# Kernel tuning notes

Hardware: AMD Instinct MI355X
Metric: run time of the kernel (lower is better)

## Reference

```python
import jax, jax.numpy as jnp
import numpy as np

B, INP, C, N, D, H = 512, 512, 1024, 256, 128, 8


def setup_inputs() -> dict:
    key = jax.random.key(0)
    ks = iter(jax.random.split(key, 40))
    rn = lambda shape, s=1.0: jax.random.normal(next(ks), shape, jnp.float32) * s
    d = {}
    d['x'] = rn((B, INP))
    d['h1'] = rn((B, C), 0.1)
    d['c1'] = rn((B, C), 0.1)
    d['h2'] = rn((B, C), 0.1)
    d['c2'] = rn((B, C), 0.1)
    d['w_prev'] = jax.nn.softmax(rn((B, H, N)), axis=-1)  # valid address dist (unused by math)
    d['r_prev'] = rn((B, H, D))
    d['M_prev'] = rn((B, N, D))
    s = 0.02
    d['W_ih1'] = rn((4 * C, INP + H * D), s); d['W_hh1'] = rn((4 * C, C), s)
    d['b_ih1'] = rn((4 * C,), s); d['b_hh1'] = rn((4 * C,), s)
    d['W_ih2'] = rn((4 * C, C), s); d['W_hh2'] = rn((4 * C, C), s)
    d['b_ih2'] = rn((4 * C,), s); d['b_hh2'] = rn((4 * C,), s)
    d['W_rk'] = rn((H * D, C), s); d['b_rk'] = rn((H * D,), s)
    d['W_wk'] = rn((H * D, C), s); d['b_wk'] = rn((H * D,), s)
    d['W_rb'] = rn((H, C), s); d['b_rb'] = rn((H,), s)
    d['W_wb'] = rn((H, C), s); d['b_wb'] = rn((H,), s)
    d['W_er'] = rn((H * D, C), s); d['b_er'] = rn((H * D,), s)
    d['W_ad'] = rn((H * D, C), s); d['b_ad'] = rn((H * D,), s)
    d['W_sh'] = rn((H * 3, C), s); d['b_sh'] = rn((H * 3,), s)
    d['W_ga'] = rn((H, C), s); d['b_ga'] = rn((H,), s)
    return d


def _lstm_cell(inp, h, c, Wih, Whh, bih, bhh):
    g = inp @ Wih.T + bih + h @ Whh.T + bhh
    i, f, gg, o = jnp.split(g, 4, axis=-1)  # torch LSTMCell gate order
    c_new = jax.nn.sigmoid(f) * c + jax.nn.sigmoid(i) * jnp.tanh(gg)
    return jax.nn.sigmoid(o) * jnp.tanh(c_new), c_new


def _normalize(v):
    n = jnp.linalg.norm(v, axis=-1, keepdims=True)
    return v / jnp.maximum(n, 1e-12)


def _content_weights(M, K, beta):
    cos = jnp.einsum('bnd,bhd->bhn', _normalize(M), _normalize(K))
    return jax.nn.softmax(beta[..., None] * cos, axis=-1)


def reference(x, h1, c1, h2, c2, w_prev, r_prev, M_prev,
              W_ih1, W_hh1, b_ih1, b_hh1, W_ih2, W_hh2, b_ih2, b_hh2,
              W_rk, b_rk, W_wk, b_wk, W_rb, b_rb, W_wb, b_wb,
              W_er, b_er, W_ad, b_ad, W_sh, b_sh, W_ga, b_ga):
    Bsz = x.shape[0]
    inp = jnp.concatenate([x, r_prev.reshape(Bsz, -1)], axis=-1)
    h1n, c1n = _lstm_cell(inp, h1, c1, W_ih1, W_hh1, b_ih1, b_hh1)
    h2n, c2n = _lstm_cell(h1n, h2, c2, W_ih2, W_hh2, b_ih2, b_hh2)  # dropout = eval identity
    RK = (h2n @ W_rk.T + b_rk).reshape(Bsz, H, D)
    WK = (h2n @ W_wk.T + b_wk).reshape(Bsz, H, D)
    Br = jax.nn.softplus(h2n @ W_rb.T + b_rb)
    Bw = jax.nn.softplus(h2n @ W_wb.T + b_wb)
    erase = jax.nn.sigmoid(h2n @ W_er.T + b_er).reshape(Bsz, H, D)
    addv = jnp.tanh(h2n @ W_ad.T + b_ad).reshape(Bsz, H, D)
    shifts = (h2n @ W_sh.T + b_sh).reshape(Bsz, H, 3)
    gamma = h2n @ W_ga.T + b_ga
    # write
    w_w = _content_weights(M_prev, WK, Bw)                      # [B,H,N]
    w_ = w_w[..., None]                                         # [B,H,N,1]
    M = M_prev * (1.0 - jnp.sum(w_ * erase[:, :, None, :], axis=1)) \
        + jnp.sum(w_ * addv[:, :, None, :], axis=1)             # [B,N,D]
    # read: content -> shift -> sharpen
    w_r = _content_weights(M, RK, Br)
    rolls = jnp.stack([jnp.roll(w_r, -1, axis=-1), w_r, jnp.roll(w_r, 1, axis=-1)], axis=-1)
    w_s = jnp.einsum('bhnk,bhk->bhn', rolls, jax.nn.softmax(shifts, axis=-1))
    g = 1.0 + jax.nn.softplus(gamma)[..., None]
    w_g = w_s ** g
    w_r = w_g / (jnp.sum(w_g, axis=-1, keepdims=True) + 1e-12)
    r = jnp.einsum('bhn,bnd->bhd', w_r, M)
    return (h1n, c1n, h2n, c2n, w_r, r, M)
```

## Files before the change

### kernel.cpp

```cpp
#include <hip/hip_runtime.h>
#include <cstdint>
#include <cstddef>


typedef __attribute__((ext_vector_type(4))) float f32x4;
typedef __attribute__((ext_vector_type(8))) __bf16 bf16x8;
typedef __attribute__((ext_vector_type(4))) unsigned short u16x4;
typedef __attribute__((ext_vector_type(8))) unsigned short u16x8;

struct ASeg { const unsigned short* A; int ldA; int kt; };
struct WSeg { const float* W; int ldW; };

__device__ __forceinline__ unsigned short f2bf(float f) {
  return __builtin_bit_cast(unsigned short, (__bf16)f);
}
__device__ __forceinline__ float sigmoidf_(float x) { return 1.f / (1.f + expf(-x)); }
__device__ __forceinline__ float softplusf_(float x) {
  return fmaxf(x, 0.f) + log1pf(expf(-fabsf(x)));
}

__device__ __forceinline__ void xcd_decode(int& k, int& g) {
  int hid = blockIdx.x;
  int xcd = hid & 7, slot = hid >> 3;
  g = xcd + 8 * (slot >> 2);
  k = slot & 3;
}


__device__ __forceinline__ void stage_tile(
    unsigned short* lAb, unsigned short* lBb,
    const float* (*s_brow)[64],
    const unsigned short* A0, int ldA0, const unsigned short* A1, int ldA1,
    const unsigned short* A2, int ldA2, int b0, int b1, int kt, int t)
{
  int si; const unsigned short* A; int ldA; int ktl;
  if (kt < b0)      { si = 0; ktl = kt;      A = A0; ldA = ldA0; }
  else if (kt < b1) { si = 1; ktl = kt - b0; A = A1; ldA = ldA1; }
  else              { si = 2; ktl = kt - b1; A = A2; ldA = ldA2; }
  const int kl = ktl * 64;
  const int wave = t >> 6, lane = t & 63;
  const int a_r8 = lane >> 3;
  const int a_col = (((lane & 7) ^ a_r8) * 8);
#pragma unroll
  for (int q = 0; q < 4; ++q) {
    const int R = (wave * 4 + q) * 8;
    const unsigned short* src = A + (size_t)(R + a_r8) * ldA + kl + a_col;
    __builtin_amdgcn_global_load_lds(
        (const __attribute__((address_space(1))) void*)src,
        (__attribute__((address_space(3))) void*)(lAb + R * 64), 16, 0, 0);
  }
  const int brow0 = t >> 4, bseg = t & 15;
#pragma unroll
  for (int i = 0; i < 4; ++i) {
    const int row = brow0 + 16 * i;
    const float* wp = s_brow[si][row];
    f32x4 v = *(const f32x4*)(wp + kl + bseg * 4);
    u16x4 p; p.x = f2bf(v.x); p.y = f2bf(v.y); p.z = f2bf(v.z); p.w = f2bf(v.w);
    *(u16x4*)&lBb[row * 64 + ((bseg * 4) ^ ((row & 7) << 3))] = p;
  }
}

__device__ __forceinline__ void mfma_tile(const unsigned short* lAb,
                                          const unsigned short* lBb,
                                          int t, f32x4 (&acc)[2][4])
{
  const int wave = t >> 6, lane = t & 63;
  const int lr = lane & 15, lk = lane >> 4;
#pragma unroll
  for (int kk = 0; kk < 2; ++kk) {
    bf16x8 af[2], bfr[4];
#pragma unroll
    for (int mi = 0; mi < 2; ++mi) {
      const int ar = wave * 32 + mi * 16 + lr;
      af[mi] = *(const bf16x8*)&lAb[ar * 64 + ((kk * 32 + lk * 8) ^ ((ar & 7) << 3))];
    }
#pragma unroll
    for (int ni = 0; ni < 4; ++ni) {
      const int br = ni * 16 + lr;
      bfr[ni] = *(const bf16x8*)&lBb[br * 64 + ((kk * 32 + lk * 8) ^ ((br & 7) << 3))];
    }
#pragma unroll
    for (int mi = 0; mi < 2; ++mi)
#pragma unroll
      for (int ni = 0; ni < 4; ++ni)
        acc[mi][ni] = __builtin_amdgcn_mfma_f32_16x16x32_bf16(af[mi], bfr[ni], acc[mi][ni], 0, 0, 0);
  }
}

#define GEMM_PIPELINE(A0, LD0, A1, LD1, A2, LD2, B0, B1, TOTAL)                    \
  stage_tile(lA[0], lB[0], s_brow, A0, LD0, A1, LD1, A2, LD2, B0, B1, 0, t);       \
  __syncthreads();                                                                 \
  _Pragma("unroll 1")                                                              \
  for (int kt = 0; kt < (TOTAL); ++kt) {                                           \
    const int cur = kt & 1;                                                        \
    if (kt + 1 < (TOTAL))                                                          \
      stage_tile(lA[cur ^ 1], lB[cur ^ 1], s_brow, A0, LD0, A1, LD1, A2, LD2,      \
                 B0, B1, kt + 1, t);                                               \
    mfma_tile(lA[cur], lB[cur], t, acc);                                           \
    __syncthreads();                                                               \
  }

__global__ __launch_bounds__(256) void lstm_gemm(
    ASeg a0, ASeg a1, ASeg a2, WSeg w0, WSeg w1, WSeg w2,
    const float* __restrict__ bih, const float* __restrict__ bhh,
    const float* __restrict__ cprev,
    float* __restrict__ hout, float* __restrict__ cout,
    unsigned short* __restrict__ hb)
{
  __shared__ __align__(16) unsigned short lA[2][128 * 64];
  __shared__ __align__(16) unsigned short lB[2][64 * 64];
  __shared__ const float* s_brow[3][64];
  const int t = threadIdx.x;
  int k, g; xcd_decode(k, g);
  const int m0 = k * 128, j0 = g * 16;

  if (t < 192) {
    const int si = t >> 6, row = t & 63;
    const float* W = si == 0 ? w0.W : si == 1 ? w1.W : w2.W;
    const int ldW  = si == 0 ? w0.ldW : si == 1 ? w1.ldW : w2.ldW;
    if (W) s_brow[si][row] = W + (size_t)((row >> 4) * 1024 + j0 + (row & 15)) * ldW;
  }
  __syncthreads();

  f32x4 acc[2][4];
#pragma unroll
  for (int i = 0; i < 2; ++i)
#pragma unroll
    for (int j = 0; j < 4; ++j) acc[i][j] = (f32x4){0.f, 0.f, 0.f, 0.f};

  const unsigned short* A0 = a0.A + (size_t)m0 * a0.ldA;
  const unsigned short* A1 = a1.A + (size_t)m0 * a1.ldA;
  const unsigned short* A2 = a2.A ? a2.A + (size_t)m0 * a2.ldA : a0.A;
  const int b0 = a0.kt, b1 = b0 + a1.kt, total = b1 + a2.kt;
  GEMM_PIPELINE(A0, a0.ldA, A1, a1.ldA, A2, a2.ldA, b0, b1, total)

  const int lane = t & 63, wave = t >> 6;
  const int lr = lane & 15, lk = lane >> 4;
  const int j = j0 + lr;
  float bs0 = bih[j] + bhh[j];
  float bs1 = bih[1024 + j] + bhh[1024 + j];
  float bs2 = bih[2048 + j] + bhh[2048 + j];
  float bs3 = bih[3072 + j] + bhh[3072 + j];
#pragma unroll
  for (int mi = 0; mi < 2; ++mi) {
#pragma unroll
    for (int jp = 0; jp < 4; ++jp) {
      const int r = m0 + wave * 32 + mi * 16 + lk * 4 + jp;
      float gi = acc[mi][0][jp] + bs0;
      float gf = acc[mi][1][jp] + bs1;
      float gc = acc[mi][2][jp] + bs2;
      float go = acc[mi][3][jp] + bs3;
      float cp = cprev[(size_t)r * 1024 + j];
      float cn = sigmoidf_(gf) * cp + sigmoidf_(gi) * tanhf(gc);
      float hn = sigmoidf_(go) * tanhf(cn);
      cout[(size_t)r * 1024 + j] = cn;
      hout[(size_t)r * 1024 + j] = hn;
      hb[(size_t)r * 1024 + j] = f2bf(hn);
    }
  }
}

__global__ __launch_bounds__(256) void heads_gemm(
    const unsigned short* __restrict__ A,
    const float* W0, const float* W1, const float* W2, const float* W3,
    const float* bb0, const float* bb1, const float* bb2, const float* bb3,
    const float* W_rb, const float* b_rb, const float* W_wb, const float* b_wb,
    const float* W_sh, const float* b_sh, const float* W_ga, const float* b_ga,
    float* o0, float* o1, float* o2, float* o3,
    float* Brw, float* Bww, float* SHw, float* GAw)
{
  __shared__ __align__(16) unsigned short lA[2][128 * 64];
  __shared__ __align__(16) unsigned short lB[2][64 * 64];
  __shared__ const float* s_brow[3][64];
  const int t = threadIdx.x;
  const bool small = (blockIdx.x >= 256);
  int m0, n0 = 0, z = 4;
  if (!small) {
    int k, g; xcd_decode(k, g);
    m0 = k * 128; n0 = (g & 15) * 64; z = g >> 4;
  } else {
    m0 = (blockIdx.x - 256) * 128;
  }
  const float* W  = z == 0 ? W0 : z == 1 ? W1 : z == 2 ? W2 : z == 3 ? W3 : nullptr;
  const float* bb = z == 0 ? bb0 : z == 1 ? bb1 : z == 2 ? bb2 : bb3;
  float* o        = z == 0 ? o0 : z == 1 ? o1 : z == 2 ? o2 : o3;

  if (t < 64) {
    if (!small) {
      s_brow[0][t] = W + (size_t)(n0 + t) * 1024;
    } else {
      const float* p;
      if (t < 8)       p = W_rb + (size_t)t * 1024;
      else if (t < 16) p = W_wb + (size_t)(t - 8) * 1024;
      else if (t < 40) p = W_sh + (size_t)(t - 16) * 1024;
      else if (t < 48) p = W_ga + (size_t)(t - 40) * 1024;
      else             p = W_ga;
      s_brow[0][t] = p;
    }
  }
  __syncthreads();

  f32x4 acc[2][4];
#pragma unroll
  for (int i = 0; i < 2; ++i)
#pragma unroll
    for (int j = 0; j < 4; ++j) acc[i][j] = (f32x4){0.f, 0.f, 0.f, 0.f};

  const unsigned short* A0 = A + (size_t)m0 * 1024;
  GEMM_PIPELINE(A0, 1024, A0, 1024, A0, 1024, 16, 16, 16)

  const int lane = t & 63, wave = t >> 6;
  const int lr = lane & 15, lk = lane >> 4;
  if (!small) {
#pragma unroll
    for (int mi = 0; mi < 2; ++mi) {
#pragma unroll
      for (int ni = 0; ni < 4; ++ni) {
        const int col = n0 + ni * 16 + lr;
        const float bv = bb[col];
#pragma unroll
        for (int jp = 0; jp < 4; ++jp) {
          const int r = m0 + wave * 32 + mi * 16 + lk * 4 + jp;
          float v = acc[mi][ni][jp] + bv;
          if (z == 2) v = sigmoidf_(v);
          else if (z == 3) v = tanhf(v);
          o[(size_t)r * 1024 + col] = v;
        }
      }
    }
  } else {
#pragma unroll
    for (int mi = 0; mi < 2; ++mi) {
#pragma unroll
      for (int ni = 0; ni < 4; ++ni) {
        const int c = ni * 16 + lr;
#pragma unroll
        for (int jp = 0; jp < 4; ++jp) {
          const int r = m0 + wave * 32 + mi * 16 + lk * 4 + jp;
          const float v = acc[mi][ni][jp];
          if (c < 8)       Brw[r * 8 + c] = softplusf_(v + b_rb[c]);
          else if (c < 16) Bww[r * 8 + (c - 8)] = softplusf_(v + b_wb[c - 8]);
          else if (c < 40) SHw[(size_t)r * 24 + (c - 16)] = v + b_sh[c - 16];
          else if (c < 48) GAw[r * 8 + (c - 40)] = v + b_ga[c - 40];
        }
      }
    }
  }
}

__global__ __launch_bounds__(256) void cvt_bf16(
    const float* __restrict__ x, const float* __restrict__ rp,
    const float* __restrict__ h1, const float* __restrict__ h2,
    unsigned short* __restrict__ ob)
{
  const int i = blockIdx.x * 256 + threadIdx.x;
  const float* src; int off;
  if (i < 32768)       { src = x;  off = i; }
  else if (i < 98304)  { src = rp; off = i - 32768; }
  else if (i < 163840) { src = h1; off = i - 98304; }
  else                 { src = h2; off = i - 163840; }
  f32x4 a = *(const f32x4*)(src + (size_t)off * 8);
  f32x4 c = *(const f32x4*)(src + (size_t)off * 8 + 4);
  u16x8 p;
  p[0] = f2bf(a.x); p[1] = f2bf(a.y); p[2] = f2bf(a.z); p[3] = f2bf(a.w);
  p[4] = f2bf(c.x); p[5] = f2bf(c.y); p[6] = f2bf(c.z); p[7] = f2bf(c.w);
  *(u16x8*)(ob + (size_t)i * 8) = p;
}

__device__ __forceinline__ void cos_pass(const float* __restrict__ Mbase,
                                         const float (*s_k)[128],
                                         const float* s_scale, float (*s_w)[256],
                                         int b, int t)
{
  const int l8 = t & 7, rg = t >> 3;
  f32x4 kv0[8], kv1[8], kv2[8], kv3[8];
#pragma unroll
  for (int h = 0; h < 8; ++h) {
    kv0[h] = *(const f32x4*)&s_k[h][(l8 + 0) * 4];
    kv1[h] = *(const f32x4*)&s_k[h][(l8 + 8) * 4];
    kv2[h] = *(const f32x4*)&s_k[h][(l8 + 16) * 4];
    kv3[h] = *(const f32x4*)&s_k[h][(l8 + 24) * 4];
  }
#pragma unroll 1
  for (int j = 0; j < 8; ++j) {
    const int n = j * 32 + rg;
    const float* mr = Mbase + ((size_t)b * 256 + n) * 128;
    f32x4 v0 = *(const f32x4*)(mr + (l8 + 0) * 4);
    f32x4 v1 = *(const f32x4*)(mr + (l8 + 8) * 4);
    f32x4 v2 = *(const f32x4*)(mr + (l8 + 16) * 4);
    f32x4 v3 = *(const f32x4*)(mr + (l8 + 24) * 4);
    f32x4 sv = v0 * v0 + v1 * v1 + v2 * v2 + v3 * v3;
    float sq = sv.x + sv.y + sv.z + sv.w;
    float dot[8];
#pragma unroll
    for (int h = 0; h < 8; ++h) {
      f32x4 dv = v0 * kv0[h] + v1 * kv1[h] + v2 * kv2[h] + v3 * kv3[h];
      dot[h] = dv.x + dv.y + dv.z + dv.w;
    }
#pragma unroll
    for (int mk = 1; mk < 8; mk <<= 1) {
      sq += __shfl_xor(sq, mk, 64);
#pragma unroll
      for (int h = 0; h < 8; ++h) dot[h] += __shfl_xor(dot[h], mk, 64);
    }
    if (l8 == 0) {
      const float invM = 1.f / fmaxf(sqrtf(sq), 1e-12f);
#pragma unroll
      for (int h = 0; h < 8; ++h) s_w[h][n] = dot[h] * invM * s_scale[h];
    }
  }
}

__device__ __forceinline__ void softmax256(float (*s_w)[256], int t) {
  const int h = t >> 5, l32 = t & 31;
  float v[8]; float mx = -3.4e38f;
#pragma unroll
  for (int i = 0; i < 8; ++i) { v[i] = s_w[h][l32 + 32 * i]; mx = fmaxf(mx, v[i]); }
#pragma unroll
  for (int mk = 1; mk < 32; mk <<= 1) mx = fmaxf(mx, __shfl_xor(mx, mk, 64));
  float sum = 0.f;
#pragma unroll
  for (int i = 0; i < 8; ++i) { v[i] = expf(v[i] - mx); sum += v[i]; }
#pragma unroll
  for (int mk = 1; mk < 32; mk <<= 1) sum += __shfl_xor(sum, mk, 64);
  const float inv = 1.f / sum;
#pragma unroll
  for (int i = 0; i < 8; ++i) s_w[h][l32 + 32 * i] = v[i] * inv;
}

__global__ __launch_bounds__(256, 2) void ntm_rw(
    const float* __restrict__ Mp, const float* __restrict__ WK,
    const float* __restrict__ ER, const float* __restrict__ AD,
    const float* __restrict__ RK,
    const float* __restrict__ Bw, const float* __restrict__ Br,
    const float* __restrict__ SH, const float* __restrict__ GA,
    float* __restrict__ Mo, float* __restrict__ wr_o, float* __restrict__ r_o)
{
  const int b = blockIdx.x, t = threadIdx.x;
  __shared__ __align__(16) float s_wk[8][128], s_er[8][128], s_ad[8][128], s_rk[8][128];
  __shared__ __align__(16) float s_w[8][256], s_w2[8][256];
  __shared__ __align__(16) float s_part[8][8][128];
  __shared__ float s_scw[8], s_scr[8], s_sh3[8][3], s_g[8];

  {
    const int h = t >> 5, d16 = (t & 31) * 4;
    const size_t off = (size_t)b * 1024 + t * 4;
    *(f32x4*)&s_wk[h][d16] = *(const f32x4*)(WK + off);
    *(f32x4*)&s_er[h][d16] = *(const f32x4*)(ER + off);
    *(f32x4*)&s_ad[h][d16] = *(const f32x4*)(AD + off);
    *(f32x4*)&s_rk[h][d16] = *(const f32x4*)(RK + off);
  }
  __syncthreads();
  if (t < 64) {
    const int h = t >> 3, l8 = t & 7;
    f32x4 aw = {0,0,0,0}, ar = {0,0,0,0};
#pragma unroll
    for (int q = 0; q < 4; ++q) {
      f32x4 w = *(const f32x4*)&s_wk[h][(l8 + q * 8) * 4];
      f32x4 r = *(const f32x4*)&s_rk[h][(l8 + q * 8) * 4];
      aw += w * w; ar += r * r;
    }
    float sw = aw.x + aw.y + aw.z + aw.w;
    float sr = ar.x + ar.y + ar.z + ar.w;
#pragma unroll
    for (int mk = 1; mk < 8; mk <<= 1) {
      sw += __shfl_xor(sw, mk, 64); sr += __shfl_xor(sr, mk, 64);
    }
    if (l8 == 0) {
      s_scw[h] = Bw[b * 8 + h] / fmaxf(sqrtf(sw), 1e-12f);
      s_scr[h] = Br[b * 8 + h] / fmaxf(sqrtf(sr), 1e-12f);
    }
  }
  if (t < 8) {
    s_g[t] = 1.f + softplusf_(GA[b * 8 + t]);
    float s0 = SH[b * 24 + t * 3], s1 = SH[b * 24 + t * 3 + 1], s2 = SH[b * 24 + t * 3 + 2];
    float mx = fmaxf(s0, fmaxf(s1, s2));
    float e0 = expf(s0 - mx), e1 = expf(s1 - mx), e2 = expf(s2 - mx);
    float inv = 1.f / (e0 + e1 + e2);
    s_sh3[t][0] = e0 * inv; s_sh3[t][1] = e1 * inv; s_sh3[t][2] = e2 * inv;
  }
  __syncthreads();

  cos_pass(Mp, s_wk, s_scw, s_w, b, t);
  __syncthreads();
  softmax256(s_w, t);
  __syncthreads();

  {
    const int d16 = (t & 31) * 4;
    f32x4 er8[8], ad8[8];
#pragma unroll
    for (int h = 0; h < 8; ++h) {
      er8[h] = *(const f32x4*)&s_er[h][d16];
      ad8[h] = *(const f32x4*)&s_ad[h][d16];
    }
#pragma unroll 1
    for (int j = 0; j < 32; ++j) {
      const int idx = j * 256 + t;
      const int n = idx >> 5;
      f32x4 m = *(const f32x4*)(Mp + (size_t)b * 32768 + (size_t)idx * 4);
      f32x4 er = {0,0,0,0}, ad = {0,0,0,0};
#pragma unroll
      for (int h = 0; h < 8; ++h) {
        const float w = s_w[h][n];
        er += w * er8[h];
        ad += w * ad8[h];
      }
      f32x4 o;
#pragma unroll
      for (int e = 0; e < 4; ++e) o[e] = m[e] * (1.f - er[e]) + ad[e];
      *(f32x4*)(Mo + (size_t)b * 32768 + (size_t)idx * 4) = o;
    }
  }
  __syncthreads();

  cos_pass(Mo, s_rk, s_scr, s_w, b, t);
  __syncthreads();
  softmax256(s_w, t);
  __syncthreads();

  {
    const int h = t >> 5, l32 = t & 31;
    float vals[8]; float sum = 0.f;
#pragma unroll
    for (int i = 0; i < 8; ++i) {
      const int n = l32 + 32 * i;
      float ws = s_w[h][(n + 1) & 255] * s_sh3[h][0]
               + s_w[h][n] * s_sh3[h][1]
               + s_w[h][(n - 1) & 255] * s_sh3[h][2];
      float wg = powf(ws, s_g[h]);
      vals[i] = wg; sum += wg;
    }
#pragma unroll
    for (int mk = 1; mk < 32; mk <<= 1) sum += __shfl_xor(sum, mk, 64);
    const float inv = 1.f / (sum + 1e-12f);
#pragma unroll
    for (int i = 0; i < 8; ++i) {
      const int n = l32 + 32 * i;
      const float w = vals[i] * inv;
      s_w2[h][n] = w;
      wr_o[((size_t)b * 8 + h) * 256 + n] = w;
    }
  }
  __syncthreads();

  {
    const int gq = t >> 5;
    const int q = t & 31;
    f32x4 pr[8];
#pragma unroll
    for (int h = 0; h < 8; ++h) pr[h] = (f32x4){0,0,0,0};
#pragma unroll 1
    for (int j = 0; j < 32; ++j) {
      const int n = j * 8 + gq;
      f32x4 v = *(const f32x4*)(Mo + (size_t)b * 32768 + (size_t)n * 128 + q * 4);
#pragma unroll
      for (int h = 0; h < 8; ++h) pr[h] += s_w2[h][n] * v;
    }
#pragma unroll
    for (int h = 0; h < 8; ++h) *(f32x4*)&s_part[gq][h][q * 4] = pr[h];
  }
  __syncthreads();
  {
    const int h = t >> 5, q = t & 31;
    f32x4 a = (f32x4){0,0,0,0};
#pragma unroll
    for (int g2 = 0; g2 < 8; ++g2) a += *(const f32x4*)&s_part[g2][h][q * 4];
    *(f32x4*)(r_o + ((size_t)b * 8 + h) * 128 + q * 4) = a;
  }
}

extern "C" void kernel_launch(void* const* d_in, const int* in_sizes, int n_in,
                              void* d_out, int out_size, void* d_ws, size_t ws_size,
                              hipStream_t stream)
{
  const float* x      = (const float*)d_in[0];
  const float* h1     = (const float*)d_in[1];
  const float* c1     = (const float*)d_in[2];
  const float* h2     = (const float*)d_in[3];
  const float* c2     = (const float*)d_in[4];
  const float* r_prev = (const float*)d_in[6];
  const float* M_prev = (const float*)d_in[7];
  const float* W_ih1  = (const float*)d_in[8];
  const float* W_hh1  = (const float*)d_in[9];
  const float* b_ih1  = (const float*)d_in[10];
  const float* b_hh1  = (const float*)d_in[11];
  const float* W_ih2  = (const float*)d_in[12];
  const float* W_hh2  = (const float*)d_in[13];
  const float* b_ih2  = (const float*)d_in[14];
  const float* b_hh2  = (const float*)d_in[15];
  const float* W_rk   = (const float*)d_in[16];
  const float* b_rk   = (const float*)d_in[17];
  const float* W_wk   = (const float*)d_in[18];
  const float* b_wk   = (const float*)d_in[19];
  const float* W_rb   = (const float*)d_in[20];
  const float* b_rb   = (const float*)d_in[21];
  const float* W_wb   = (const float*)d_in[22];
  const float* b_wb   = (const float*)d_in[23];
  const float* W_er   = (const float*)d_in[24];
  const float* b_er   = (const float*)d_in[25];
  const float* W_ad   = (const float*)d_in[26];
  const float* b_ad   = (const float*)d_in[27];
  const float* W_sh   = (const float*)d_in[28];
  const float* b_sh   = (const float*)d_in[29];
  const float* W_ga   = (const float*)d_in[30];
  const float* b_ga   = (const float*)d_in[31];

  float* out = (float*)d_out;
  float* h1n = out;
  float* c1n = out + 524288;
  float* h2n = out + 1048576;
  float* c2n = out + 1572864;
  float* wro = out + 2097152;
  float* r_o = out + 3145728;
  float* M_o = out + 3670016;

  float* wsf = (float*)d_ws;
  float* RK  = wsf;
  float* WKb = RK + 524288;
  float* ER  = WKb + 524288;
  float* AD  = ER + 524288;
  float* Brb = AD + 524288;
  float* Bwb = Brb + 4096;
  float* SHb = Bwb + 4096;
  float* GAb = SHb + 12288;
  const size_t f32_need  = 2121728;
  const size_t bf16_need = 2883584;
  unsigned short* bfb;
  if (ws_size >= f32_need * 4 + bf16_need * 2) {
    bfb = (unsigned short*)(wsf + f32_need);
  } else {
    bfb = (unsigned short*)(M_o + (16777216 - (bf16_need + 1) / 2));
  }
  unsigned short* xb   = bfb;
  unsigned short* rb   = xb + 262144;
  unsigned short* h1b  = rb + 524288;
  unsigned short* h2b  = h1b + 524288;
  unsigned short* h1nb = h2b + 524288;
  unsigned short* h2nb = h1nb + 524288;

  cvt_bf16<<<896, 256, 0, stream>>>(x, r_prev, h1, h2, xb);

  ASeg a0{xb, 512, 8}, a1{rb, 1024, 16}, a2{h1b, 1024, 16};
  WSeg w0{W_ih1, 1536}, w1{W_ih1 + 512, 1536}, w2{W_hh1, 1024};
  lstm_gemm<<<256, 256, 0, stream>>>(a0, a1, a2, w0, w1, w2,
                                     b_ih1, b_hh1, c1, h1n, c1n, h1nb);

  ASeg d0{h1nb, 1024, 16}, d1{h2b, 1024, 16}, d2{nullptr, 0, 0};
  WSeg v0{W_ih2, 1024}, v1{W_hh2, 1024}, v2{nullptr, 0};
  lstm_gemm<<<256, 256, 0, stream>>>(d0, d1, d2, v0, v1, v2,
                                     b_ih2, b_hh2, c2, h2n, c2n, h2nb);

  heads_gemm<<<260, 256, 0, stream>>>(h2nb, W_rk, W_wk, W_er, W_ad,
                                      b_rk, b_wk, b_er, b_ad,
                                      W_rb, b_rb, W_wb, b_wb, W_sh, b_sh, W_ga, b_ga,
                                      RK, WKb, ER, AD, Brb, Bwb, SHb, GAb);

  ntm_rw<<<512, 256, 0, stream>>>(M_prev, WKb, ER, AD, RK, Bwb, Brb, SHb, GAb,
                                  M_o, wro, r_o);
}
```

Measured before the change: 522.3 us.

## Split-K LSTM GEMMs with smaller tiles and separate fused cell kernel

The LSTM gate GEMMs move to 64x64 tiles with a two-way split-K, going from 256 to 1024 blocks. They write raw gate partials to workspace, and a new elementwise lstm_cell kernel sums the partials, adds biases and applies the cell nonlinearities. The heads GEMM also uses 64-row tiles and twice as many blocks, and the ntm_rw loops are unrolled to issue several memory loads before use. The goal is more blocks in flight on a GPU that was underfilled and better hiding of memory latency. In exchange it adds extra global traffic for the gate partials, two more kernel launches, and less reuse of the weight tiles.

```diff
diff --git a/kernel.cpp b/kernel.cpp
--- a/kernel.cpp
+++ b/kernel.cpp
@@ -19,15 +19,14 @@
   return fmaxf(x, 0.f) + log1pf(expf(-fabsf(x)));
 }
 
-__device__ __forceinline__ void xcd_decode(int& k, int& g) {
-  int hid = blockIdx.x;
+__device__ __forceinline__ void xcd_decode512(int hid, int& k, int& g) {
   int xcd = hid & 7, slot = hid >> 3;
-  g = xcd + 8 * (slot >> 2);
-  k = slot & 3;
-}
-
-
-__device__ __forceinline__ void stage_tile(
+  g = xcd + 8 * (slot >> 3);
+  k = slot & 7;
+}
+
+
+__device__ __forceinline__ void stage_tile64(
     unsigned short* lAb, unsigned short* lBb,
     const float* (*s_brow)[64],
     const unsigned short* A0, int ldA0, const unsigned short* A1, int ldA1,
@@ -42,8 +41,8 @@
   const int a_r8 = lane >> 3;
   const int a_col = (((lane & 7) ^ a_r8) * 8);
 #pragma unroll
-  for (int q = 0; q < 4; ++q) {
-    const int R = (wave * 4 + q) * 8;
+  for (int q = 0; q < 2; ++q) {
+    const int R = (wave * 2 + q) * 8;
     const unsigned short* src = A + (size_t)(R + a_r8) * ldA + kl + a_col;
     __builtin_amdgcn_global_load_lds(
         (const __attribute__((address_space(1))) void*)src,
@@ -60,107 +59,121 @@
   }
 }
 
-__device__ __forceinline__ void mfma_tile(const unsigned short* lAb,
-                                          const unsigned short* lBb,
-                                          int t, f32x4 (&acc)[2][4])
+__device__ __forceinline__ void mfma_tile64(const unsigned short* lAb,
+                                            const unsigned short* lBb,
+                                            int t, f32x4 (&acc)[4])
 {
   const int wave = t >> 6, lane = t & 63;
   const int lr = lane & 15, lk = lane >> 4;
 #pragma unroll
   for (int kk = 0; kk < 2; ++kk) {
-    bf16x8 af[2], bfr[4];
-#pragma unroll
-    for (int mi = 0; mi < 2; ++mi) {
-      const int ar = wave * 32 + mi * 16 + lr;
-      af[mi] = *(const bf16x8*)&lAb[ar * 64 + ((kk * 32 + lk * 8) ^ ((ar & 7) << 3))];
-    }
+    const int ar = wave * 16 + lr;
+    bf16x8 af = *(const bf16x8*)&lAb[ar * 64 + ((kk * 32 + lk * 8) ^ ((ar & 7) << 3))];
+    bf16x8 bfr[4];
 #pragma unroll
     for (int ni = 0; ni < 4; ++ni) {
       const int br = ni * 16 + lr;
       bfr[ni] = *(const bf16x8*)&lBb[br * 64 + ((kk * 32 + lk * 8) ^ ((br & 7) << 3))];
     }
 #pragma unroll
-    for (int mi = 0; mi < 2; ++mi)
-#pragma unroll
-      for (int ni = 0; ni < 4; ++ni)
-        acc[mi][ni] = __builtin_amdgcn_mfma_f32_16x16x32_bf16(af[mi], bfr[ni], acc[mi][ni], 0, 0, 0);
-  }
-}
-
-#define GEMM_PIPELINE(A0, LD0, A1, LD1, A2, LD2, B0, B1, TOTAL)                    \
-  stage_tile(lA[0], lB[0], s_brow, A0, LD0, A1, LD1, A2, LD2, B0, B1, 0, t);       \
+    for (int ni = 0; ni < 4; ++ni)
+      acc[ni] = __builtin_amdgcn_mfma_f32_16x16x32_bf16(af, bfr[ni], acc[ni], 0, 0, 0);
+  }
+}
+
+#define GEMM_PIPELINE64(A0, LD0, A1, LD1, A2, LD2, B0, B1, KB, KE)                 \
+  stage_tile64(lA[0], lB[0], s_brow, A0, LD0, A1, LD1, A2, LD2, B0, B1, KB, t);    \
   __syncthreads();                                                                 \
   _Pragma("unroll 1")                                                              \
-  for (int kt = 0; kt < (TOTAL); ++kt) {                                           \
-    const int cur = kt & 1;                                                        \
-    if (kt + 1 < (TOTAL))                                                          \
-      stage_tile(lA[cur ^ 1], lB[cur ^ 1], s_brow, A0, LD0, A1, LD1, A2, LD2,      \
-                 B0, B1, kt + 1, t);                                               \
-    mfma_tile(lA[cur], lB[cur], t, acc);                                           \
+  for (int kt = (KB); kt < (KE); ++kt) {                                           \
+    const int cur = (kt - (KB)) & 1;                                               \
+    if (kt + 1 < (KE))                                                             \
+      stage_tile64(lA[cur ^ 1], lB[cur ^ 1], s_brow, A0, LD0, A1, LD1, A2, LD2,    \
+                   B0, B1, kt + 1, t);                                             \
+    mfma_tile64(lA[cur], lB[cur], t, acc);                                         \
     __syncthreads();                                                               \
   }
 
-__global__ __launch_bounds__(256) void lstm_gemm(
+__global__ __launch_bounds__(256, 4) void lstm_gemm(
     ASeg a0, ASeg a1, ASeg a2, WSeg w0, WSeg w1, WSeg w2,
+    float* __restrict__ g0out, float* __restrict__ g1out, int khalf, int ktotal)
+{
+  __shared__ __align__(16) unsigned short lA[2][64 * 64];
+  __shared__ __align__(16) unsigned short lB[2][64 * 64];
+  __shared__ const float* s_brow[3][64];
+  const int t = threadIdx.x;
+  const int hid = blockIdx.x;
+  const int split = hid >> 9;
+  int k, g; xcd_decode512(hid & 511, k, g);
+  const int m0 = k * 64, n0 = g * 64;
+  const int kb = split ? khalf : 0, ke = split ? ktotal : khalf;
+  float* gout = split ? g1out : g0out;
+
+  if (t < 192) {
+    const int si = t >> 6, row = t & 63;
+    const float* W = si == 0 ? w0.W : si == 1 ? w1.W : w2.W;
+    const int ldW  = si == 0 ? w0.ldW : si == 1 ? w1.ldW : w2.ldW;
+    if (W) s_brow[si][row] = W + (size_t)(n0 + row) * ldW;
+  }
+  __syncthreads();
+
+  f32x4 acc[4];
+#pragma unroll
+  for (int j = 0; j < 4; ++j) acc[j] = (f32x4){0.f, 0.f, 0.f, 0.f};
+
+  const unsigned short* A0 = a0.A + (size_t)m0 * a0.ldA;
+  const unsigned short* A1 = a1.A + (size_t)m0 * a1.ldA;
+  const unsigned short* A2 = a2.A ? a2.A + (size_t)m0 * a2.ldA : a0.A;
+  const int b0 = a0.kt, b1 = b0 + a1.kt;
+  GEMM_PIPELINE64(A0, a0.ldA, A1, a1.ldA, A2, a2.ldA, b0, b1, kb, ke)
+
+  const int lane = t & 63, wave = t >> 6;
+  const int lr = lane & 15, lk = lane >> 4;
+#pragma unroll
+  for (int ni = 0; ni < 4; ++ni) {
+    const int col = n0 + ni * 16 + lr;
+#pragma unroll
+    for (int jp = 0; jp < 4; ++jp) {
+      const int r = m0 + wave * 16 + lk * 4 + jp;
+      gout[(size_t)r * 4096 + col] = acc[ni][jp];
+    }
+  }
+}
+
+__global__ __launch_bounds__(256) void lstm_cell(
+    const float* __restrict__ g0, const float* __restrict__ g1,
     const float* __restrict__ bih, const float* __restrict__ bhh,
     const float* __restrict__ cprev,
     float* __restrict__ hout, float* __restrict__ cout,
     unsigned short* __restrict__ hb)
 {
-  __shared__ __align__(16) unsigned short lA[2][128 * 64];
-  __shared__ __align__(16) unsigned short lB[2][64 * 64];
-  __shared__ const float* s_brow[3][64];
-  const int t = threadIdx.x;
-  int k, g; xcd_decode(k, g);
-  const int m0 = k * 128, j0 = g * 16;
-
-  if (t < 192) {
-    const int si = t >> 6, row = t & 63;
-    const float* W = si == 0 ? w0.W : si == 1 ? w1.W : w2.W;
-    const int ldW  = si == 0 ? w0.ldW : si == 1 ? w1.ldW : w2.ldW;
-    if (W) s_brow[si][row] = W + (size_t)((row >> 4) * 1024 + j0 + (row & 15)) * ldW;
-  }
-  __syncthreads();
-
-  f32x4 acc[2][4];
-#pragma unroll
-  for (int i = 0; i < 2; ++i)
-#pragma unroll
-    for (int j = 0; j < 4; ++j) acc[i][j] = (f32x4){0.f, 0.f, 0.f, 0.f};
-
-  const unsigned short* A0 = a0.A + (size_t)m0 * a0.ldA;
-  const unsigned short* A1 = a1.A + (size_t)m0 * a1.ldA;
-  const unsigned short* A2 = a2.A ? a2.A + (size_t)m0 * a2.ldA : a0.A;
-  const int b0 = a0.kt, b1 = b0 + a1.kt, total = b1 + a2.kt;
-  GEMM_PIPELINE(A0, a0.ldA, A1, a1.ldA, A2, a2.ldA, b0, b1, total)
-
-  const int lane = t & 63, wave = t >> 6;
-  const int lr = lane & 15, lk = lane >> 4;
-  const int j = j0 + lr;
-  float bs0 = bih[j] + bhh[j];
-  float bs1 = bih[1024 + j] + bhh[1024 + j];
-  float bs2 = bih[2048 + j] + bhh[2048 + j];
-  float bs3 = bih[3072 + j] + bhh[3072 + j];
-#pragma unroll
-  for (int mi = 0; mi < 2; ++mi) {
-#pragma unroll
-    for (int jp = 0; jp < 4; ++jp) {
-      const int r = m0 + wave * 32 + mi * 16 + lk * 4 + jp;
-      float gi = acc[mi][0][jp] + bs0;
-      float gf = acc[mi][1][jp] + bs1;
-      float gc = acc[mi][2][jp] + bs2;
-      float go = acc[mi][3][jp] + bs3;
-      float cp = cprev[(size_t)r * 1024 + j];
-      float cn = sigmoidf_(gf) * cp + sigmoidf_(gi) * tanhf(gc);
-      float hn = sigmoidf_(go) * tanhf(cn);
-      cout[(size_t)r * 1024 + j] = cn;
-      hout[(size_t)r * 1024 + j] = hn;
-      hb[(size_t)r * 1024 + j] = f2bf(hn);
-    }
-  }
-}
-
-__global__ __launch_bounds__(256) void heads_gemm(
+  const int idx = blockIdx.x * 256 + threadIdx.x;
+  const int b = idx >> 8, j4 = idx & 255;
+  const int j = j4 * 4;
+  const float* ga = g0 + (size_t)b * 4096;
+  const float* gb = g1 + (size_t)b * 4096;
+  f32x4 gi = *(const f32x4*)(ga + j)        + *(const f32x4*)(gb + j)
+           + *(const f32x4*)(bih + j)        + *(const f32x4*)(bhh + j);
+  f32x4 gf = *(const f32x4*)(ga + 1024 + j) + *(const f32x4*)(gb + 1024 + j)
+           + *(const f32x4*)(bih + 1024 + j) + *(const f32x4*)(bhh + 1024 + j);
+  f32x4 gc = *(const f32x4*)(ga + 2048 + j) + *(const f32x4*)(gb + 2048 + j)
+           + *(const f32x4*)(bih + 2048 + j) + *(const f32x4*)(bhh + 2048 + j);
+  f32x4 go = *(const f32x4*)(ga + 3072 + j) + *(const f32x4*)(gb + 3072 + j)
+           + *(const f32x4*)(bih + 3072 + j) + *(const f32x4*)(bhh + 3072 + j);
+  f32x4 c = *(const f32x4*)(cprev + (size_t)idx * 4);
+  f32x4 cn, hn; u16x4 hp;
+#pragma unroll
+  for (int e = 0; e < 4; ++e) {
+    float cne = sigmoidf_(gf[e]) * c[e] + sigmoidf_(gi[e]) * tanhf(gc[e]);
+    float hne = sigmoidf_(go[e]) * tanhf(cne);
+    cn[e] = cne; hn[e] = hne; hp[e] = f2bf(hne);
+  }
+  *(f32x4*)(cout + (size_t)idx * 4) = cn;
+  *(f32x4*)(hout + (size_t)idx * 4) = hn;
+  *(u16x4*)(hb + (size_t)idx * 4) = hp;
+}
+
+__global__ __launch_bounds__(256, 4) void heads_gemm(
     const unsigned short* __restrict__ A,
     const float* W0, const float* W1, const float* W2, const float* W3,
     const float* bb0, const float* bb1, const float* bb2, const float* bb3,
@@ -169,17 +182,18 @@
     float* o0, float* o1, float* o2, float* o3,
     float* Brw, float* Bww, float* SHw, float* GAw)
 {
-  __shared__ __align__(16) unsigned short lA[2][128 * 64];
+  __shared__ __align__(16) unsigned short lA[2][64 * 64];
   __shared__ __align__(16) unsigned short lB[2][64 * 64];
   __shared__ const float* s_brow[3][64];
   const int t = threadIdx.x;
-  const bool small = (blockIdx.x >= 256);
+  const int hid = blockIdx.x;
+  const bool small = (hid >= 512);
   int m0, n0 = 0, z = 4;
   if (!small) {
-    int k, g; xcd_decode(k, g);
-    m0 = k * 128; n0 = (g & 15) * 64; z = g >> 4;
+    int k, g; xcd_decode512(hid, k, g);
+    m0 = k * 64; n0 = (g & 15) * 64; z = g >> 4;
   } else {
-    m0 = (blockIdx.x - 256) * 128;
+    m0 = (hid - 512) * 64;
   }
   const float* W  = z == 0 ? W0 : z == 1 ? W1 : z == 2 ? W2 : z == 3 ? W3 : nullptr;
   const float* bb = z == 0 ? bb0 : z == 1 ? bb1 : z == 2 ? bb2 : bb3;
@@ -200,49 +214,41 @@
   }
   __syncthreads();
 
-  f32x4 acc[2][4];
-#pragma unroll
-  for (int i = 0; i < 2; ++i)
-#pragma unroll
-    for (int j = 0; j < 4; ++j) acc[i][j] = (f32x4){0.f, 0.f, 0.f, 0.f};
+  f32x4 acc[4];
+#pragma unroll
+  for (int j = 0; j < 4; ++j) acc[j] = (f32x4){0.f, 0.f, 0.f, 0.f};
 
   const unsigned short* A0 = A + (size_t)m0 * 1024;
-  GEMM_PIPELINE(A0, 1024, A0, 1024, A0, 1024, 16, 16, 16)
+  GEMM_PIPELINE64(A0, 1024, A0, 1024, A0, 1024, 16, 16, 0, 16)
 
   const int lane = t & 63, wave = t >> 6;
   const int lr = lane & 15, lk = lane >> 4;
   if (!small) {
 #pragma unroll
-    for (int mi = 0; mi < 2; ++mi) {
-#pragma unroll
-      for (int ni = 0; ni < 4; ++ni) {
-        const int col = n0 + ni * 16 + lr;
-        const float bv = bb[col];
-#pragma unroll
-        for (int jp = 0; jp < 4; ++jp) {
-          const int r = m0 + wave * 32 + mi * 16 + lk * 4 + jp;
-          float v = acc[mi][ni][jp] + bv;
-          if (z == 2) v = sigmoidf_(v);
-          else if (z == 3) v = tanhf(v);
-          o[(size_t)r * 1024 + col] = v;
-        }
+    for (int ni = 0; ni < 4; ++ni) {
+      const int col = n0 + ni * 16 + lr;
+      const float bv = bb[col];
+#pragma unroll
+      for (int jp = 0; jp < 4; ++jp) {
+        const int r = m0 + wave * 16 + lk * 4 + jp;
+        float v = acc[ni][jp] + bv;
+        if (z == 2) v = sigmoidf_(v);
+        else if (z == 3) v = tanhf(v);
+        o[(size_t)r * 1024 + col] = v;
       }
     }
   } else {
 #pragma unroll
-    for (int mi = 0; mi < 2; ++mi) {
-#pragma unroll
-      for (int ni = 0; ni < 4; ++ni) {
-        const int c = ni * 16 + lr;
-#pragma unroll
-        for (int jp = 0; jp < 4; ++jp) {
-          const int r = m0 + wave * 32 + mi * 16 + lk * 4 + jp;
-          const float v = acc[mi][ni][jp];
-          if (c < 8)       Brw[r * 8 + c] = softplusf_(v + b_rb[c]);
-          else if (c < 16) Bww[r * 8 + (c - 8)] = softplusf_(v + b_wb[c - 8]);
-          else if (c < 40) SHw[(size_t)r * 24 + (c - 16)] = v + b_sh[c - 16];
-          else if (c < 48) GAw[r * 8 + (c - 40)] = v + b_ga[c - 40];
-        }
+    for (int ni = 0; ni < 4; ++ni) {
+      const int c = ni * 16 + lr;
+#pragma unroll
+      for (int jp = 0; jp < 4; ++jp) {
+        const int r = m0 + wave * 16 + lk * 4 + jp;
+        const float v = acc[ni][jp];
+        if (c < 8)       Brw[r * 8 + c] = softplusf_(v + b_rb[c]);
+        else if (c < 16) Bww[r * 8 + (c - 8)] = softplusf_(v + b_wb[c - 8]);
+        else if (c < 40) SHw[(size_t)r * 24 + (c - 16)] = v + b_sh[c - 16];
+        else if (c < 48) GAw[r * 8 + (c - 40)] = v + b_ga[c - 40];
       }
     }
   }
@@ -282,31 +288,48 @@
     kv3[h] = *(const f32x4*)&s_k[h][(l8 + 24) * 4];
   }
 #pragma unroll 1
-  for (int j = 0; j < 8; ++j) {
-    const int n = j * 32 + rg;
-    const float* mr = Mbase + ((size_t)b * 256 + n) * 128;
-    f32x4 v0 = *(const f32x4*)(mr + (l8 + 0) * 4);
-    f32x4 v1 = *(const f32x4*)(mr + (l8 + 8) * 4);
-    f32x4 v2 = *(const f32x4*)(mr + (l8 + 16) * 4);
-    f32x4 v3 = *(const f32x4*)(mr + (l8 + 24) * 4);
-    f32x4 sv = v0 * v0 + v1 * v1 + v2 * v2 + v3 * v3;
-    float sq = sv.x + sv.y + sv.z + sv.w;
-    float dot[8];
+  for (int jo = 0; jo < 4; ++jo) {
+    const int na = jo * 64 + rg, nb = na + 32;
+    const float* mra = Mbase + ((size_t)b * 256 + na) * 128;
+    const float* mrb = Mbase + ((size_t)b * 256 + nb) * 128;
+    f32x4 a0 = *(const f32x4*)(mra + (l8 + 0) * 4);
+    f32x4 a1 = *(const f32x4*)(mra + (l8 + 8) * 4);
+    f32x4 a2 = *(const f32x4*)(mra + (l8 + 16) * 4);
+    f32x4 a3 = *(const f32x4*)(mra + (l8 + 24) * 4);
+    f32x4 c0 = *(const f32x4*)(mrb + (l8 + 0) * 4);
+    f32x4 c1 = *(const f32x4*)(mrb + (l8 + 8) * 4);
+    f32x4 c2 = *(const f32x4*)(mrb + (l8 + 16) * 4);
+    f32x4 c3 = *(const f32x4*)(mrb + (l8 + 24) * 4);
+    f32x4 sa = a0 * a0 + a1 * a1 + a2 * a2 + a3 * a3;
+    f32x4 sb = c0 * c0 + c1 * c1 + c2 * c2 + c3 * c3;
+    float sqa = sa.x + sa.y + sa.z + sa.w;
+    float sqb = sb.x + sb.y + sb.z + sb.w;
+    float dota[8], dotb[8];
 #pragma unroll
     for (int h = 0; h < 8; ++h) {
-      f32x4 dv = v0 * kv0[h] + v1 * kv1[h] + v2 * kv2[h] + v3 * kv3[h];
-      dot[h] = dv.x + dv.y + dv.z + dv.w;
+      f32x4 da = a0 * kv0[h] + a1 * kv1[h] + a2 * kv2[h] + a3 * kv3[h];
+      f32x4 db = c0 * kv0[h] + c1 * kv1[h] + c2 * kv2[h] + c3 * kv3[h];
+      dota[h] = da.x + da.y + da.z + da.w;
+      dotb[h] = db.x + db.y + db.z + db.w;
     }
 #pragma unroll
     for (int mk = 1; mk < 8; mk <<= 1) {
-      sq += __shfl_xor(sq, mk, 64);
-#pragma unroll
-      for (int h = 0; h < 8; ++h) dot[h] += __shfl_xor(dot[h], mk, 64);
+      sqa += __shfl_xor(sqa, mk, 64);
+      sqb += __shfl_xor(sqb, mk, 64);
+#pragma unroll
+      for (int h = 0; h < 8; ++h) {
+        dota[h] += __shfl_xor(dota[h], mk, 64);
+        dotb[h] += __shfl_xor(dotb[h], mk, 64);
+      }
     }
     if (l8 == 0) {
-      const float invM = 1.f / fmaxf(sqrtf(sq), 1e-12f);
-#pragma unroll
-      for (int h = 0; h < 8; ++h) s_w[h][n] = dot[h] * invM * s_scale[h];
+      const float ia = 1.f / fmaxf(sqrtf(sqa), 1e-12f);
+      const float ib = 1.f / fmaxf(sqrtf(sqb), 1e-12f);
+#pragma unroll
+      for (int h = 0; h < 8; ++h) {
+        s_w[h][na] = dota[h] * ia * s_scale[h];
+        s_w[h][nb] = dotb[h] * ib * s_scale[h];
+      }
     }
   }
 }
@@ -395,21 +418,29 @@
       ad8[h] = *(const f32x4*)&s_ad[h][d16];
     }
 #pragma unroll 1
-    for (int j = 0; j < 32; ++j) {
-      const int idx = j * 256 + t;
-      const int n = idx >> 5;
-      f32x4 m = *(const f32x4*)(Mp + (size_t)b * 32768 + (size_t)idx * 4);
-      f32x4 er = {0,0,0,0}, ad = {0,0,0,0};
-#pragma unroll
-      for (int h = 0; h < 8; ++h) {
-        const float w = s_w[h][n];
-        er += w * er8[h];
-        ad += w * ad8[h];
+    for (int jo = 0; jo < 8; ++jo) {
+      const int idx0 = jo * 1024 + t;
+      f32x4 m0v = *(const f32x4*)(Mp + (size_t)b * 32768 + (size_t)(idx0 + 0) * 4);
+      f32x4 m1v = *(const f32x4*)(Mp + (size_t)b * 32768 + (size_t)(idx0 + 256) * 4);
+      f32x4 m2v = *(const f32x4*)(Mp + (size_t)b * 32768 + (size_t)(idx0 + 512) * 4);
+      f32x4 m3v = *(const f32x4*)(Mp + (size_t)b * 32768 + (size_t)(idx0 + 768) * 4);
+      f32x4 mv[4] = {m0v, m1v, m2v, m3v};
+#pragma unroll
+      for (int i = 0; i < 4; ++i) {
+        const int idx = idx0 + i * 256;
+        const int n = idx >> 5;
+        f32x4 er = {0,0,0,0}, ad = {0,0,0,0};
+#pragma unroll
+        for (int h = 0; h < 8; ++h) {
+          const float w = s_w[h][n];
+          er += w * er8[h];
+          ad += w * ad8[h];
+        }
+        f32x4 o;
+#pragma unroll
+        for (int e = 0; e < 4; ++e) o[e] = mv[i][e] * (1.f - er[e]) + ad[e];
+        *(f32x4*)(Mo + (size_t)b * 32768 + (size_t)idx * 4) = o;
       }
-      f32x4 o;
-#pragma unroll
-      for (int e = 0; e < 4; ++e) o[e] = m[e] * (1.f - er[e]) + ad[e];
-      *(f32x4*)(Mo + (size_t)b * 32768 + (size_t)idx * 4) = o;
     }
   }
   __syncthreads();
@@ -445,17 +476,24 @@
   __syncthreads();
 
   {
-    const int gq = t >> 5;
-    const int q = t & 31;
+    const int gq = t >> 5, q = t & 31;
     f32x4 pr[8];
 #pragma unroll
     for (int h = 0; h < 8; ++h) pr[h] = (f32x4){0,0,0,0};
 #pragma unroll 1
-    for (int j = 0; j < 32; ++j) {
-      const int n = j * 8 + gq;
-      f32x4 v = *(const f32x4*)(Mo + (size_t)b * 32768 + (size_t)n * 128 + q * 4);
-#pragma unroll
-      for (int h = 0; h < 8; ++h) pr[h] += s_w2[h][n] * v;
+    for (int jo = 0; jo < 8; ++jo) {
+      const int nb0 = jo * 32 + gq;
+      f32x4 v0 = *(const f32x4*)(Mo + (size_t)b * 32768 + (size_t)(nb0 + 0)  * 128 + q * 4);
+      f32x4 v1 = *(const f32x4*)(Mo + (size_t)b * 32768 + (size_t)(nb0 + 8)  * 128 + q * 4);
+      f32x4 v2 = *(const f32x4*)(Mo + (size_t)b * 32768 + (size_t)(nb0 + 16) * 128 + q * 4);
+      f32x4 v3 = *(const f32x4*)(Mo + (size_t)b * 32768 + (size_t)(nb0 + 24) * 128 + q * 4);
+      f32x4 vv[4] = {v0, v1, v2, v3};
+#pragma unroll
+      for (int i = 0; i < 4; ++i) {
+        const int n = nb0 + i * 8;
+#pragma unroll
+        for (int h = 0; h < 8; ++h) pr[h] += s_w2[h][n] * vv[i];
+      }
     }
 #pragma unroll
     for (int h = 0; h < 8; ++h) *(f32x4*)&s_part[gq][h][q * 4] = pr[h];
@@ -524,13 +562,18 @@
   float* Bwb = Brb + 4096;
   float* SHb = Bwb + 4096;
   float* GAb = SHb + 12288;
-  const size_t f32_need  = 2121728;
-  const size_t bf16_need = 2883584;
-  unsigned short* bfb;
-  if (ws_size >= f32_need * 4 + bf16_need * 2) {
-    bfb = (unsigned short*)(wsf + f32_need);
+  const size_t head_f32   = 2121728;
+  const size_t gates_f32  = 2 * 2097152;
+  const size_t bf16_elems = 2883584;
+  float* g0; float* g1; unsigned short* bfb;
+  if (ws_size >= (head_f32 + gates_f32) * 4 + bf16_elems * 2) {
+    g0 = wsf + head_f32;
+    g1 = g0 + 2097152;
+    bfb = (unsigned short*)(g1 + 2097152);
   } else {
-    bfb = (unsigned short*)(M_o + (16777216 - (bf16_need + 1) / 2));
+    g0 = M_o;
+    g1 = M_o + 2097152;
+    bfb = (unsigned short*)(M_o + (16777216 - (bf16_elems + 1) / 2));
   }
   unsigned short* xb   = bfb;
   unsigned short* rb   = xb + 262144;
@@ -543,15 +586,15 @@
 
   ASeg a0{xb, 512, 8}, a1{rb, 1024, 16}, a2{h1b, 1024, 16};
   WSeg w0{W_ih1, 1536}, w1{W_ih1 + 512, 1536}, w2{W_hh1, 1024};
-  lstm_gemm<<<256, 256, 0, stream>>>(a0, a1, a2, w0, w1, w2,
-                                     b_ih1, b_hh1, c1, h1n, c1n, h1nb);
+  lstm_gemm<<<1024, 256, 0, stream>>>(a0, a1, a2, w0, w1, w2, g0, g1, 20, 40);
+  lstm_cell<<<512, 256, 0, stream>>>(g0, g1, b_ih1, b_hh1, c1, h1n, c1n, h1nb);
 
   ASeg d0{h1nb, 1024, 16}, d1{h2b, 1024, 16}, d2{nullptr, 0, 0};
   WSeg v0{W_ih2, 1024}, v1{W_hh2, 1024}, v2{nullptr, 0};
-  lstm_gemm<<<256, 256, 0, stream>>>(d0, d1, d2, v0, v1, v2,
-                                     b_ih2, b_hh2, c2, h2n, c2n, h2nb);
-
-  heads_gemm<<<260, 256, 0, stream>>>(h2nb, W_rk, W_wk, W_er, W_ad,
+  lstm_gemm<<<1024, 256, 0, stream>>>(d0, d1, d2, v0, v1, v2, g0, g1, 16, 32);
+  lstm_cell<<<512, 256, 0, stream>>>(g0, g1, b_ih2, b_hh2, c2, h2n, c2n, h2nb);
+
+  heads_gemm<<<520, 256, 0, stream>>>(h2nb, W_rk, W_wk, W_er, W_ad,
                                       b_rk, b_wk, b_er, b_ad,
                                       W_rb, b_rb, W_wb, b_wb, W_sh, b_sh, W_ga, b_ga,
                                       RK, WKb, ER, AD, Brb, Bwb, SHb, GAb);
```

New measurement: 457.3 us. -12.4%, faster.
